# Performance work log

Hardware: AMD Instinct MI355X
Metric: run time of the kernel (lower is better)

Reference implementation:

```python
import jax, jax.numpy as jnp
import numpy as np

LR = 0.01            # learning_rate
PC = 0.001           # pred_clipping
WC = 5.0             # weight_clipping
_LO = float(np.log(PC / (1.0 - PC)))   # logit(pred_clipping)
_HI = -_LO                              # logit(1 - pred_clipping)


def setup_inputs() -> dict:
    B, S, I, CTX, M, C = 64, 1023, 1024, 784, 4, 1  # S = size-1 (bias row), C = num_classes->1
    key = jax.random.key(0)
    k = jax.random.split(key, 6)
    logit = jax.random.normal(k[0], (B, I, C), jnp.float32)
    context = jax.random.normal(k[1], (B, CTX), jnp.float32)
    target = jax.random.uniform(k[2], (B, C), dtype=jnp.float32)
    cm = jax.random.normal(k[3], (C, S, M, CTX), jnp.float32)
    cm = cm / jnp.linalg.norm(cm, axis=-1, keepdims=True)          # unit-norm context maps
    cb = jax.random.normal(k[4], (C, S, M, 1), jnp.float32)        # context bias
    weights = jnp.full((C, S, 2 ** M, I), 1.0 / I, jnp.float32)    # per-context weight table
    bias = jax.random.uniform(k[5], (1, 1, C), jnp.float32, _LO, _HI)
    return {"logit": logit, "context": context, "target": target,
            "context_maps": cm, "context_bias": cb, "weights": weights, "bias": bias}


def reference(logit, context, target, context_maps, context_bias, weights, bias):
    C, S, M, _ = context_maps.shape
    B = context.shape[0]
    # halfspace hashing of the context -> per-(class, neuron, sample) weight-table index
    dist = jnp.einsum('csmk,bk->csmb', context_maps, context)      # [C,S,M,B]
    bits = (dist > context_bias).astype(jnp.int32)
    conv = (2 ** jnp.arange(M, dtype=jnp.int32))[:, None]          # [M,1]
    idx = jnp.sum(bits * conv, axis=-2)                            # [C,S,B] in [0, 2^M)
    ci = jnp.arange(C)[:, None, None]
    si = jnp.arange(S)[None, :, None]
    sel = weights[ci, si, idx]                                     # gather -> [C,S,B,I]
    # batched dot product (torch code does full matmul + diagonal; this is the same math)
    out = jnp.clip(jnp.einsum('csbi,bic->csb', sel, logit), _LO, _HI)
    out_bsc = out.transpose(2, 1, 0)                               # [B,S,C]
    # online weight update (target branch): gather-compute-scatter
    diff = jax.nn.sigmoid(out_bsc) - target[:, None, :]            # [B,S,C]
    upd = LR * diff[..., None] * logit.transpose(0, 2, 1)[:, None, :, :]  # [B,S,C,I]
    new_sel = jnp.clip(sel - upd.transpose(2, 1, 0, 3), -WC, WC)   # [C,S,B,I]
    new_weights = weights.at[ci, si, idx].set(new_sel)             # scatter
    # prepend constant bias neuron
    out_logits = jnp.concatenate([jnp.broadcast_to(bias, (B, 1, C)), out_bsc], axis=1)  # [B,S+1,C]
    return out_logits, new_weights
```

## Files before the change

### kernel.cpp

```cpp
#include <hip/hip_runtime.h>
#include <math.h>

typedef unsigned long long u64;
typedef __attribute__((ext_vector_type(8))) short bf16x8;
typedef __attribute__((ext_vector_type(4))) float f32x4;

#define S_DIM 1023
#define B_DIM 64
#define I_DIM 1024
#define CTX_DIM 784
#define CTX4 196
#define NWROWS 16

#define LR_C 0.01f
#define WC_C 5.0f
#define LO_C (-6.906754778648554f)
#define HI_C ( 6.906754778648554f)

__device__ __forceinline__ float dot4(float4 a, float4 b) {
    return a.x * b.x + a.y * b.y + a.z * b.z + a.w * b.w;
}

__device__ __forceinline__ float4 upd4(float4 w, float4 a, float c) {
    float4 r;
    r.x = fminf(fmaxf(w.x - c * a.x, -WC_C), WC_C);
    r.y = fminf(fmaxf(w.y - c * a.y, -WC_C), WC_C);
    r.z = fminf(fmaxf(w.z - c * a.z, -WC_C), WC_C);
    r.w = fminf(fmaxf(w.w - c * a.w, -WC_C), WC_C);
    return r;
}

__device__ __forceinline__ short f2bf(float f) {
    union { float f; unsigned u; } cv; cv.f = f;
    unsigned r = cv.u + 0x7fffu + ((cv.u >> 16) & 1u);
    return (short)(r >> 16);
}

__global__ __launch_bounds__(256) void prep_kernel(
    const float* __restrict__ context,
    const float* __restrict__ bias,
    float4* __restrict__ ctxT4,
    float* __restrict__ out_logits)
{
    int g = blockIdx.x * 256 + threadIdx.x;
    int k4 = g >> 6;
    int b  = g & 63;
    ctxT4[g] = *(const float4*)(context + (size_t)b * CTX_DIM + k4 * 4);
    if (g < B_DIM) out_logits[(size_t)g * (S_DIM + 1)] = bias[0];
}

__global__ __launch_bounds__(256) void pack_kernel(
    const float* __restrict__ logit,
    short* __restrict__ pack_b)
{
    int g = blockIdx.x * 256 + threadIdx.x;
    int l  = g & 63;
    int kb = (g >> 6) & 31;
    int nt = g >> 11;
    int b  = nt * 16 + (l & 15);
    int i0 = kb * 32 + (l >> 4) * 8;
    const float* src = logit + (size_t)b * I_DIM + i0;
    bf16x8 v;
    #pragma unroll
    for (int j = 0; j < 8; ++j) v[j] = f2bf(src[j]);
    *(bf16x8*)(pack_b + (size_t)g * 8) = v;
}

__global__ __launch_bounds__(256, 4) void gln_fused_kernel(
    const float* __restrict__ logit,
    const float* __restrict__ target,
    const float* __restrict__ weights,
    const float* __restrict__ cm,
    const float* __restrict__ cb,
    const float4* __restrict__ ctxT4,
    const short* __restrict__ pack_b,
    float* __restrict__ out_logits,
    float* __restrict__ new_weights)
{
    __shared__ short Abf[NWROWS * I_DIM];
    __shared__ float red[4][4][64];
    __shared__ int   bits[4][64];
    __shared__ float cb_lds[4];
    __shared__ u64   mask_lds[NWROWS];
    __shared__ int   lastb_lds[NWROWS];
    __shared__ float coef_lds[NWROWS];

    const int s  = blockIdx.x;
    const int t  = threadIdx.x;
    const int wv = t >> 6;
    const int l  = t & 63;

    const float4* W4 = (const float4*)(weights + (size_t)s * (NWROWS * I_DIM));
    float4 Wr[16];
    #pragma unroll
    for (int j = 0; j < 16; ++j) Wr[j] = W4[t + j * 256];

    if (t < 4) cb_lds[t] = cb[s * 4 + t];

    {
        const int b = t & 63;
        const int q = __builtin_amdgcn_readfirstlane(t >> 6);
        const float4* cmr = (const float4*)(cm + (size_t)s * 4 * CTX_DIM);
        float a0 = 0.f, a1 = 0.f, a2 = 0.f, a3 = 0.f;
        const int k0 = q * 49;
        #pragma unroll 7
        for (int kk = 0; kk < 49; ++kk) {
            int k4 = k0 + kk;
            float4 c4 = ctxT4[k4 * 64 + b];
            a0 += dot4(cmr[k4], c4);
            a1 += dot4(cmr[CTX4 + k4], c4);
            a2 += dot4(cmr[2 * CTX4 + k4], c4);
            a3 += dot4(cmr[3 * CTX4 + k4], c4);
        }
        red[q][0][b] = a0;
        red[q][1][b] = a1;
        red[q][2][b] = a2;
        red[q][3][b] = a3;
    }
    __syncthreads();
    {
        int m = t >> 6, bb = t & 63;
        float sum = red[0][m][bb] + red[1][m][bb] + red[2][m][bb] + red[3][m][bb];
        bits[m][bb] = (sum > cb_lds[m]) ? 1 : 0;
    }
    __syncthreads();
    if (t < B_DIM) {
        int v = bits[0][t] + 2 * bits[1][t] + 4 * bits[2][t] + 8 * bits[3][t];
        u64 my = 0;
        #pragma unroll
        for (int kk = 0; kk < NWROWS; ++kk) {
            u64 mk = __ballot(v == kk);
            if (t == kk) my = mk;
        }
        if (t < NWROWS) {
            mask_lds[t]  = my;
            lastb_lds[t] = my ? (63 - __clzll(my)) : -1;
        }
    }

    #pragma unroll
    for (int j = 0; j < 16; ++j) {
        int slot = j * 128 + ((t >> 1) ^ (j & 7));
        short4 v;
        v.x = f2bf(Wr[j].x); v.y = f2bf(Wr[j].y);
        v.z = f2bf(Wr[j].z); v.w = f2bf(Wr[j].w);
        *(short4*)(Abf + slot * 8 + (t & 1) * 4) = v;
    }
    __syncthreads();

    const int row = l & 15;
    const int q2  = l >> 4;
    const int sw  = row & 7;
    const int base_slot = row * 128;
    const bf16x8* Bb = (const bf16x8*)pack_b + (size_t)wv * 2048 + l;
    f32x4 acc = {0.f, 0.f, 0.f, 0.f};
    #pragma unroll 8
    for (int kb = 0; kb < 32; ++kb) {
        bf16x8 af = *(const bf16x8*)(Abf + 8 * (base_slot + ((kb * 4 + q2) ^ sw)));
        bf16x8 bfr = Bb[(size_t)kb * 64];
        acc = __builtin_amdgcn_mfma_f32_16x16x32_bf16(af, bfr, acc, 0, 0, 0);
    }

    const int col = wv * 16 + (l & 15);
    #pragma unroll
    for (int j = 0; j < 4; ++j) {
        int r = q2 * 4 + j;
        u64 m = mask_lds[r];
        if ((m >> col) & 1) {
            float o = fminf(fmaxf(acc[j], LO_C), HI_C);
            out_logits[(size_t)col * (S_DIM + 1) + s + 1] = o;
            if (col == lastb_lds[r])
                coef_lds[r] = LR_C * (1.0f / (1.0f + expf(-o)) - target[col]);
        }
    }
    __syncthreads();

    float4*       D4 = (float4*)(new_weights + (size_t)s * (NWROWS * I_DIM));
    const float4* L4 = (const float4*)logit;
    #pragma unroll
    for (int r = 0; r < NWROWS; ++r) {
        const int lb = lastb_lds[r];
        float4 o;
        if (lb < 0) {
            o = Wr[r];
        } else {
            o = upd4(Wr[r], L4[lb * 256 + t], coef_lds[r]);
        }
        D4[r * 256 + t] = o;
    }
}

extern "C" void kernel_launch(void* const* d_in, const int* in_sizes, int n_in,
                              void* d_out, int out_size, void* d_ws, size_t ws_size,
                              hipStream_t stream) {
    const float* logit   = (const float*)d_in[0];
    const float* context = (const float*)d_in[1];
    const float* target  = (const float*)d_in[2];
    const float* cm      = (const float*)d_in[3];
    const float* cb      = (const float*)d_in[4];
    const float* weights = (const float*)d_in[5];
    const float* bias    = (const float*)d_in[6];

    float* out_logits  = (float*)d_out;
    float* new_weights = out_logits + (size_t)B_DIM * (S_DIM + 1);

    char* ws = (char*)d_ws;
    float4* ctxT4 = (float4*)ws;     ws += (size_t)CTX4 * B_DIM * 16;
    short*  packb = (short*)ws;

    prep_kernel<<<CTX4 * B_DIM / 256, 256, 0, stream>>>(context, bias, ctxT4, out_logits);
    pack_kernel<<<32, 256, 0, stream>>>(logit, packb);
    gln_fused_kernel<<<S_DIM, 256, 0, stream>>>(logit, target, weights, cm, cb,
                                                ctxT4, packb, out_logits, new_weights);
}
```

Measured before the change: 58.81 us.

## Merge prep kernels, drop weight register cache, and interleave staging with hashing

Merges the context-transpose and logit-pack kernels into one launch to save a kernel launch. The main kernel no longer holds 16 float4 weight values in registers across the whole body; it converts them straight to bf16 in LDS and re-reads them from global memory in the final update loop. Odd and even blocks run the weight staging and the context-hash reduction in opposite orders so that memory traffic and ALU work from different blocks overlap. The cost is a second global read of each block's weight tile (64 KB per block), in exchange for lower register pressure and possibly higher occupancy.

```diff
diff --git a/kernel.cpp b/kernel.cpp
--- a/kernel.cpp
+++ b/kernel.cpp
@@ -36,37 +36,38 @@
     return (short)(r >> 16);
 }
 
-__global__ __launch_bounds__(256) void prep_kernel(
+__global__ __launch_bounds__(256) void prep_pack_kernel(
     const float* __restrict__ context,
     const float* __restrict__ bias,
+    const float* __restrict__ logit,
     float4* __restrict__ ctxT4,
+    short* __restrict__ pack_b,
     float* __restrict__ out_logits)
 {
-    int g = blockIdx.x * 256 + threadIdx.x;
-    int k4 = g >> 6;
-    int b  = g & 63;
-    ctxT4[g] = *(const float4*)(context + (size_t)b * CTX_DIM + k4 * 4);
-    if (g < B_DIM) out_logits[(size_t)g * (S_DIM + 1)] = bias[0];
-}
-
-__global__ __launch_bounds__(256) void pack_kernel(
-    const float* __restrict__ logit,
-    short* __restrict__ pack_b)
-{
-    int g = blockIdx.x * 256 + threadIdx.x;
-    int l  = g & 63;
-    int kb = (g >> 6) & 31;
-    int nt = g >> 11;
-    int b  = nt * 16 + (l & 15);
-    int i0 = kb * 32 + (l >> 4) * 8;
-    const float* src = logit + (size_t)b * I_DIM + i0;
-    bf16x8 v;
-    #pragma unroll
-    for (int j = 0; j < 8; ++j) v[j] = f2bf(src[j]);
-    *(bf16x8*)(pack_b + (size_t)g * 8) = v;
-}
-
-__global__ __launch_bounds__(256, 4) void gln_fused_kernel(
+    const int blk = blockIdx.x;
+    const int t = threadIdx.x;
+    if (blk < 49) {
+        int g = blk * 256 + t;
+        int k4 = g >> 6;
+        int b  = g & 63;
+        ctxT4[g] = *(const float4*)(context + (size_t)b * CTX_DIM + k4 * 4);
+        if (g < B_DIM) out_logits[(size_t)g * (S_DIM + 1)] = bias[0];
+    } else {
+        int g = (blk - 49) * 256 + t;
+        int l  = g & 63;
+        int kb = (g >> 6) & 31;
+        int nt = g >> 11;
+        int b  = nt * 16 + (l & 15);
+        int i0 = kb * 32 + (l >> 4) * 8;
+        const float* src = logit + (size_t)b * I_DIM + i0;
+        bf16x8 v;
+        #pragma unroll
+        for (int j = 0; j < 8; ++j) v[j] = f2bf(src[j]);
+        *(bf16x8*)(pack_b + (size_t)g * 8) = v;
+    }
+}
+
+__global__ __launch_bounds__(256, 4) void gln_all_kernel(
     const float* __restrict__ logit,
     const float* __restrict__ target,
     const float* __restrict__ weights,
@@ -90,34 +91,47 @@
     const int wv = t >> 6;
     const int l  = t & 63;
 
+    if (t < 4) cb_lds[t] = cb[s * 4 + t];
+
     const float4* W4 = (const float4*)(weights + (size_t)s * (NWROWS * I_DIM));
-    float4 Wr[16];
-    #pragma unroll
-    for (int j = 0; j < 16; ++j) Wr[j] = W4[t + j * 256];
-
-    if (t < 4) cb_lds[t] = cb[s * 4 + t];
-
-    {
-        const int b = t & 63;
-        const int q = __builtin_amdgcn_readfirstlane(t >> 6);
-        const float4* cmr = (const float4*)(cm + (size_t)s * 4 * CTX_DIM);
-        float a0 = 0.f, a1 = 0.f, a2 = 0.f, a3 = 0.f;
-        const int k0 = q * 49;
-        #pragma unroll 7
-        for (int kk = 0; kk < 49; ++kk) {
-            int k4 = k0 + kk;
-            float4 c4 = ctxT4[k4 * 64 + b];
-            a0 += dot4(cmr[k4], c4);
-            a1 += dot4(cmr[CTX4 + k4], c4);
-            a2 += dot4(cmr[2 * CTX4 + k4], c4);
-            a3 += dot4(cmr[3 * CTX4 + k4], c4);
-        }
-        red[q][0][b] = a0;
-        red[q][1][b] = a1;
-        red[q][2][b] = a2;
-        red[q][3][b] = a3;
-    }
-    __syncthreads();
+
+    #define DO_STAGE() do {                                            \
+        _Pragma("unroll")                                              \
+        for (int j = 0; j < 16; ++j) {                                 \
+            float4 w = W4[t + j * 256];                                \
+            int slot = j * 128 + ((t >> 1) ^ (j & 7));                 \
+            short4 v;                                                  \
+            v.x = f2bf(w.x); v.y = f2bf(w.y);                          \
+            v.z = f2bf(w.z); v.w = f2bf(w.w);                          \
+            *(short4*)(Abf + slot * 8 + (t & 1) * 4) = v;              \
+        }                                                              \
+    } while (0)
+
+    #define DO_IDXRED() do {                                           \
+        const int b = t & 63;                                          \
+        const int q = __builtin_amdgcn_readfirstlane(t >> 6);          \
+        const float4* cmr = (const float4*)(cm + (size_t)s * 4 * CTX_DIM); \
+        float a0 = 0.f, a1 = 0.f, a2 = 0.f, a3 = 0.f;                  \
+        const int k0 = q * 49;                                         \
+        _Pragma("unroll 7")                                            \
+        for (int kk = 0; kk < 49; ++kk) {                              \
+            int k4 = k0 + kk;                                          \
+            float4 c4 = ctxT4[k4 * 64 + b];                            \
+            a0 += dot4(cmr[k4], c4);                                   \
+            a1 += dot4(cmr[CTX4 + k4], c4);                            \
+            a2 += dot4(cmr[2 * CTX4 + k4], c4);                        \
+            a3 += dot4(cmr[3 * CTX4 + k4], c4);                        \
+        }                                                              \
+        red[q][0][b] = a0;                                             \
+        red[q][1][b] = a1;                                             \
+        red[q][2][b] = a2;                                             \
+        red[q][3][b] = a3;                                             \
+    } while (0)
+
+    if (s & 1) { DO_STAGE(); DO_IDXRED(); }
+    else       { DO_IDXRED(); DO_STAGE(); }
+    __syncthreads();
+
     {
         int m = t >> 6, bb = t & 63;
         float sum = red[0][m][bb] + red[1][m][bb] + red[2][m][bb] + red[3][m][bb];
@@ -136,15 +150,6 @@
             mask_lds[t]  = my;
             lastb_lds[t] = my ? (63 - __clzll(my)) : -1;
         }
-    }
-
-    #pragma unroll
-    for (int j = 0; j < 16; ++j) {
-        int slot = j * 128 + ((t >> 1) ^ (j & 7));
-        short4 v;
-        v.x = f2bf(Wr[j].x); v.y = f2bf(Wr[j].y);
-        v.z = f2bf(Wr[j].z); v.w = f2bf(Wr[j].w);
-        *(short4*)(Abf + slot * 8 + (t & 1) * 4) = v;
     }
     __syncthreads();
 
@@ -177,14 +182,15 @@
 
     float4*       D4 = (float4*)(new_weights + (size_t)s * (NWROWS * I_DIM));
     const float4* L4 = (const float4*)logit;
-    #pragma unroll
+    #pragma unroll 8
     for (int r = 0; r < NWROWS; ++r) {
         const int lb = lastb_lds[r];
+        float4 w = W4[r * 256 + t];
         float4 o;
         if (lb < 0) {
-            o = Wr[r];
+            o = w;
         } else {
-            o = upd4(Wr[r], L4[lb * 256 + t], coef_lds[r]);
+            o = upd4(w, L4[lb * 256 + t], coef_lds[r]);
         }
         D4[r * 256 + t] = o;
     }
@@ -208,8 +214,7 @@
     float4* ctxT4 = (float4*)ws;     ws += (size_t)CTX4 * B_DIM * 16;
     short*  packb = (short*)ws;
 
-    prep_kernel<<<CTX4 * B_DIM / 256, 256, 0, stream>>>(context, bias, ctxT4, out_logits);
-    pack_kernel<<<32, 256, 0, stream>>>(logit, packb);
-    gln_fused_kernel<<<S_DIM, 256, 0, stream>>>(logit, target, weights, cm, cb,
-                                                ctxT4, packb, out_logits, new_weights);
-}
+    prep_pack_kernel<<<81, 256, 0, stream>>>(context, bias, logit, ctxT4, packb, out_logits);
+    gln_all_kernel<<<S_DIM, 256, 0, stream>>>(logit, target, weights, cm, cb,
+                                              ctxT4, packb, out_logits, new_weights);
+}
```

Result: no change. 59.58 us (+1.3%).
